# Kernel optimization log

Measured on AMD Instinct MI355X. Metric: run time of the kernel, lower is better.

Reference implementation:

```python
import jax, jax.numpy as jnp
import numpy as np

N_NODES = 50000

def gcn_conv(x, src, dst, W, b, n_nodes):
    # PyG GCNConv: add self-loops, symmetric deg^{-1/2} normalization,
    # linear transform, scatter-add aggregation (source -> target), bias.
    loop = jnp.arange(n_nodes, dtype=src.dtype)
    src2 = jnp.concatenate([src, loop])
    dst2 = jnp.concatenate([dst, loop])
    deg = jax.ops.segment_sum(jnp.ones_like(dst2, dtype=x.dtype), dst2, num_segments=n_nodes)
    dinv = jnp.where(deg > 0, jax.lax.rsqrt(deg), 0.0)
    norm = dinv[src2] * dinv[dst2]  # [E + N]
    h = x @ W                        # [N, out]
    msg = h[src2] * norm[:, None]    # gather + scale
    out = jax.ops.segment_sum(msg, dst2, num_segments=n_nodes)
    return out + b

def setup_inputs() -> dict:
    key = jax.random.key(0)
    k1, k2, k3, k4 = jax.random.split(key, 4)
    x = jax.random.normal(k1, (N_NODES, 64), dtype=jnp.float32)
    edge_index = jax.random.randint(k2, (2, 800000), 0, N_NODES, dtype=jnp.int64)
    # Glorot-ish init for weights
    W1 = jax.random.normal(k3, (64, 128), dtype=jnp.float32) * (1.0 / np.sqrt(64))
    b1 = jnp.zeros((128,), dtype=jnp.float32)
    W2 = jax.random.normal(k4, (128, 8), dtype=jnp.float32) * (1.0 / np.sqrt(128))
    b2 = jnp.zeros((8,), dtype=jnp.float32)
    return {"x": x, "edge_index": edge_index, "W1": W1, "b1": b1, "W2": W2, "b2": b2}

def reference(x, edge_index, W1, b1, W2, b2):
    src, dst = edge_index[0], edge_index[1]
    h = gcn_conv(x, src, dst, W1, b1, N_NODES)
    h = jax.nn.relu(h)
    out = gcn_conv(h, src, dst, W2, b2, N_NODES)
    return out
```

## Files before the change

### kernel.cpp

```cpp
#include <hip/hip_runtime.h>

#define IN1 64
#define MID 128
#define OUT2 8
#define YPAD 136
#define TPAD 68
#define CAP 64

__device__ __forceinline__ unsigned short f2bf(float f) {
    unsigned int u = __float_as_uint(f);
    unsigned int r = (u + 0x7fff + ((u >> 16) & 1)) >> 16;
    return (unsigned short)r;
}
__device__ __forceinline__ float bflo(unsigned int u) { return __uint_as_float(u << 16); }
__device__ __forceinline__ float bfhi(unsigned int u) { return __uint_as_float(u & 0xffff0000u); }

__global__ __launch_bounds__(256) void k_xb(const float4* __restrict__ x4,
                                            ushort4* __restrict__ xb4,
                                            int* __restrict__ cnt, int n16, int N) {
    int gid = blockIdx.x * 256 + (int)threadIdx.x;
    if (gid < N) cnt[gid] = 0;
    if (gid >= n16) return;
    float4 vx = x4[gid];
    ushort4 pv;
    pv.x = f2bf(vx.x); pv.y = f2bf(vx.y);
    pv.z = f2bf(vx.z); pv.w = f2bf(vx.w);
    xb4[gid] = pv;
}

__global__ __launch_bounds__(256) void k_fill(const int* __restrict__ src,
                                              const int* __restrict__ dst,
                                              int* __restrict__ cnt,
                                              unsigned short* __restrict__ col,
                                              int E4, int E, int npx, int slices) {
    int xcd = blockIdx.x & 7;
    int slice = blockIdx.x >> 3;
    int lo = xcd * npx, hi = lo + npx;
    int eps = (E4 + slices - 1) / slices;
    int g0 = slice * eps, g1 = min(E4, g0 + eps);
    int g = g0 + (int)threadIdx.x;
    if (g < g1) {
        int4 dv = ((const int4*)dst)[g];
        int4 sv = ((const int4*)src)[g];
        for (;;) {
            int gn = g + 256;
            bool has = gn < g1;
            int4 dn, sn;
            if (has) { dn = ((const int4*)dst)[gn]; sn = ((const int4*)src)[gn]; }
            if (dv.x >= lo && dv.x < hi) {
                int p = atomicAdd(&cnt[dv.x], 1);
                if (p < CAP) col[dv.x * CAP + p] = (unsigned short)sv.x;
            }
            if (dv.y >= lo && dv.y < hi) {
                int p = atomicAdd(&cnt[dv.y], 1);
                if (p < CAP) col[dv.y * CAP + p] = (unsigned short)sv.y;
            }
            if (dv.z >= lo && dv.z < hi) {
                int p = atomicAdd(&cnt[dv.z], 1);
                if (p < CAP) col[dv.z * CAP + p] = (unsigned short)sv.z;
            }
            if (dv.w >= lo && dv.w < hi) {
                int p = atomicAdd(&cnt[dv.w], 1);
                if (p < CAP) col[dv.w * CAP + p] = (unsigned short)sv.w;
            }
            if (!has) break;
            dv = dn; sv = sn;
            g = gn;
        }
    }
    if (blockIdx.x == 0 && threadIdx.x == 0) {
        for (int e = E4 * 4; e < E; ++e) {
            int d = dst[e];
            int p = atomicAdd(&cnt[d], 1);
            if (p < CAP) col[d * CAP + p] = (unsigned short)src[e];
        }
    }
}

__global__ __launch_bounds__(256) void k_node(const uint4* __restrict__ xb4,
                                              const int* __restrict__ cnt,
                                              const unsigned short* __restrict__ col,
                                              const float* __restrict__ W1,
                                              const float* __restrict__ b1,
                                              const float* __restrict__ W2,
                                              float* __restrict__ z, int n) {
    __shared__ float w2s[MID * OUT2];
    __shared__ float tS[4][8][TPAD];
    __shared__ float yS[4][8][YPAD];

    int t = threadIdx.x;
    ((float4*)w2s)[t] = ((const float4*)W2)[t];

    int lane = t & 63, wave = t >> 6;
    int g = lane >> 3;
    int fl = lane & 7;
    int row0 = blockIdx.x * 32 + wave * 8;
    int row = row0 + g;
    bool valid = row < n;

    float a0=0.f,a1=0.f,a2=0.f,a3=0.f,a4=0.f,a5=0.f,a6=0.f,a7=0.f;
    int deg = 0, base = 0;
    if (valid) {
        int c0 = cnt[row];
        deg = min(c0, CAP);
        base = row * CAP;
        float dself = rsqrtf((float)(c0 + 1));
        uint4 u = xb4[(size_t)row * 8 + fl];
        a0 = dself * bflo(u.x); a1 = dself * bfhi(u.x);
        a2 = dself * bflo(u.y); a3 = dself * bfhi(u.y);
        a4 = dself * bflo(u.z); a5 = dself * bfhi(u.z);
        a6 = dself * bflo(u.w); a7 = dself * bfhi(u.w);
    }
    int cv = (deg >= 8) ? col[base + fl] : 0;
    float dsv = rsqrtf((float)(cnt[cv] + 1));
    int j = 0;
    for (; j + 8 <= deg; j += 8) {
        int cvn = (j + 16 <= deg) ? col[base + j + 8 + fl] : 0;
        float dsn = rsqrtf((float)(cnt[cvn] + 1));
#pragma unroll
        for (int p = 0; p < 8; ++p) {
            int sl = (g << 3) + p;
            int s = __shfl(cv, sl, 64);
            float ds = __shfl(dsv, sl, 64);
            uint4 u = xb4[(size_t)s * 8 + fl];
            a0 = fmaf(ds, bflo(u.x), a0); a1 = fmaf(ds, bfhi(u.x), a1);
            a2 = fmaf(ds, bflo(u.y), a2); a3 = fmaf(ds, bfhi(u.y), a3);
            a4 = fmaf(ds, bflo(u.z), a4); a5 = fmaf(ds, bfhi(u.z), a5);
            a6 = fmaf(ds, bflo(u.w), a6); a7 = fmaf(ds, bfhi(u.w), a7);
        }
        cv = cvn; dsv = dsn;
    }
    int rem = deg - j;
    if (rem > 0) {
        int cvr = col[base + min(j + fl, CAP - 1)];
        float dsr = rsqrtf((float)(cnt[cvr] + 1));
#pragma unroll
        for (int p = 0; p < 8; ++p) {
            if (p < rem) {
                int sl = (g << 3) + p;
                int s = __shfl(cvr, sl, 64);
                float ds = __shfl(dsr, sl, 64);
                uint4 u = xb4[(size_t)s * 8 + fl];
                a0 = fmaf(ds, bflo(u.x), a0); a1 = fmaf(ds, bfhi(u.x), a1);
                a2 = fmaf(ds, bflo(u.y), a2); a3 = fmaf(ds, bfhi(u.y), a3);
                a4 = fmaf(ds, bflo(u.z), a4); a5 = fmaf(ds, bfhi(u.z), a5);
                a6 = fmaf(ds, bflo(u.w), a6); a7 = fmaf(ds, bfhi(u.w), a7);
            }
        }
    }
    {
        float4 w0 = {a0, a1, a2, a3};
        float4 w1v = {a4, a5, a6, a7};
        *(float4*)&tS[wave][g][8 * fl] = w0;
        *(float4*)&tS[wave][g][8 * fl + 4] = w1v;
    }

    float dnd[8];
#pragma unroll
    for (int k = 0; k < 8; ++k) {
        int ck = cnt[min(row0 + k, n - 1)];
        dnd[k] = rsqrtf((float)(ck + 1));
    }

    float ya[8], yb[8];
#pragma unroll
    for (int i = 0; i < 8; ++i) { ya[i] = 0.f; yb[i] = 0.f; }
#pragma unroll 2
    for (int k4 = 0; k4 < IN1; k4 += 4) {
        float4 tv[8];
#pragma unroll
        for (int nd = 0; nd < 8; ++nd) tv[nd] = *(const float4*)&tS[wave][nd][k4];
#pragma unroll
        for (int kk = 0; kk < 4; ++kk) {
            int k = k4 + kk;
            float wa = W1[k * MID + lane];
            float wb = W1[k * MID + lane + 64];
#pragma unroll
            for (int nd = 0; nd < 8; ++nd) {
                float e = (&tv[nd].x)[kk];
                ya[nd] = fmaf(e, wa, ya[nd]);
                yb[nd] = fmaf(e, wb, yb[nd]);
            }
        }
    }
    float bl = b1[lane], bh = b1[lane + 64];
#pragma unroll
    for (int nd = 0; nd < 8; ++nd) {
        yS[wave][nd][lane] = fmaxf(fmaf(ya[nd], dnd[nd], bl), 0.f);
        yS[wave][nd][lane + 64] = fmaxf(fmaf(yb[nd], dnd[nd], bh), 0.f);
    }

    __syncthreads();

    int nd2 = lane >> 3, ch = lane & 7;
    float p[OUT2];
#pragma unroll
    for (int c = 0; c < OUT2; ++c) p[c] = 0.0f;
#pragma unroll
    for (int kk = 0; kk < 16; ++kk) {
        int k = kk * 8 + ch;
        float yk = yS[wave][nd2][k];
        float4 wlo = *(const float4*)&w2s[k * OUT2];
        float4 whi = *(const float4*)&w2s[k * OUT2 + 4];
        p[0] = fmaf(yk, wlo.x, p[0]); p[1] = fmaf(yk, wlo.y, p[1]);
        p[2] = fmaf(yk, wlo.z, p[2]); p[3] = fmaf(yk, wlo.w, p[3]);
        p[4] = fmaf(yk, whi.x, p[4]); p[5] = fmaf(yk, whi.y, p[5]);
        p[6] = fmaf(yk, whi.z, p[6]); p[7] = fmaf(yk, whi.w, p[7]);
    }
#pragma unroll
    for (int off = 1; off < 8; off <<= 1) {
#pragma unroll
        for (int c = 0; c < OUT2; ++c) p[c] += __shfl_xor(p[c], off, 64);
    }
    int rw = row0 + nd2;
    if (rw < n) {
        z[(size_t)rw * OUT2 + ch] = p[ch] * dnd[nd2];
    }
}

__global__ __launch_bounds__(256) void k_gather2(const int* __restrict__ cnt,
                                                 const unsigned short* __restrict__ col,
                                                 const float* __restrict__ z,
                                                 const float* __restrict__ b2,
                                                 float* __restrict__ out, int n) {
    int t = threadIdx.x, lane = t & 63, wave = t >> 6;
    int node = blockIdx.x * 4 + wave;
    if (node >= n) return;
    int nb = lane >> 3, c = lane & 7;
    float acc = (nb == 0) ? z[(size_t)node * OUT2 + c] : 0.0f;
    int c0 = cnt[node];
    int deg = min(c0, CAP);
    int base = node * CAP;
    int j = nb;
    if (j + 8 < deg) {
        int s0 = col[base + j], s1 = col[base + j + 8];
        for (; j + 8 < deg;) {
            int jn = j + 16;
            int t0 = 0, t1 = 0;
            bool has = jn + 8 < deg;
            if (has) { t0 = col[base + jn]; t1 = col[base + jn + 8]; }
            acc += z[(size_t)s0 * OUT2 + c] + z[(size_t)s1 * OUT2 + c];
            j = jn;
            if (!has) break;
            s0 = t0; s1 = t1;
        }
    }
    if (j < deg) acc += z[(size_t)col[base + j] * OUT2 + c];
#pragma unroll
    for (int off = 8; off < 64; off <<= 1) acc += __shfl_xor(acc, off, 64);
    if (lane < OUT2) out[(size_t)node * OUT2 + lane] = fmaf(acc, rsqrtf((float)(c0 + 1)), b2[lane]);
}

extern "C" void kernel_launch(void* const* d_in, const int* in_sizes, int n_in,
                              void* d_out, int out_size, void* d_ws, size_t ws_size,
                              hipStream_t stream) {
    const float* x  = (const float*)d_in[0];
    const int*   ei = (const int*)d_in[1];
    const float* W1 = (const float*)d_in[2];
    const float* b1 = (const float*)d_in[3];
    const float* W2 = (const float*)d_in[4];
    const float* b2 = (const float*)d_in[5];
    float* out = (float*)d_out;

    int N = in_sizes[0] / IN1;
    int E = in_sizes[1] / 2;
    const int* src = ei;
    const int* dst = ei + E;

    int* cnt = (int*)d_ws;
    unsigned short* col = (unsigned short*)(cnt + N);
    float* z = (float*)(col + (size_t)N * CAP);
    unsigned short* xb = (unsigned short*)(z + (size_t)N * OUT2);

    const int B = 256;
    int E4 = E / 4;
    int npx = (N + 7) / 8;
    int slices = 256;
    int n16 = N * 16;

    k_xb<<<(n16 + B - 1) / B, B, 0, stream>>>((const float4*)x, (ushort4*)xb, cnt, n16, N);
    k_fill<<<slices * 8, B, 0, stream>>>(src, dst, cnt, col, E4, E, npx, slices);
    k_node<<<(N + 31) / 32, 256, 0, stream>>>((const uint4*)xb, cnt, col, W1, b1, W2, z, N);
    k_gather2<<<(N + 3) / 4, 256, 0, stream>>>(cnt, col, z, b2, out, N);
}
```

Measured before the change: 170.9 us.

## Precompute degree normalization in fill kernel and simplify gather loop

The last block per XCD slice of the fill kernel, found with an atomic done counter, computes dinv = rsqrt(cnt+1) for its node range. The node and gather kernels then read dinv directly instead of recomputing rsqrt from cnt for every neighbor. The shuffle-based software prefetch of neighbor indices in the aggregation loop is replaced by direct per-neighbor col and dinv loads. W2 is now read from global memory instead of shared memory, which lets the block-wide barrier go, and YPAD shrinks. In exchange it adds an atomic and threadfence at the end of the fill kernel, and it may lose the latency hiding the old prefetch provided.

```diff
diff --git a/kernel.cpp b/kernel.cpp
--- a/kernel.cpp
+++ b/kernel.cpp
@@ -3,7 +3,7 @@
 #define IN1 64
 #define MID 128
 #define OUT2 8
-#define YPAD 136
+#define YPAD 132
 #define TPAD 68
 #define CAP 64
 
@@ -17,9 +17,11 @@
 
 __global__ __launch_bounds__(256) void k_xb(const float4* __restrict__ x4,
                                             ushort4* __restrict__ xb4,
-                                            int* __restrict__ cnt, int n16, int N) {
+                                            int* __restrict__ cnt,
+                                            int* __restrict__ done, int n16, int N) {
     int gid = blockIdx.x * 256 + (int)threadIdx.x;
     if (gid < N) cnt[gid] = 0;
+    if (gid < 8) done[gid] = 0;
     if (gid >= n16) return;
     float4 vx = x4[gid];
     ushort4 pv;
@@ -32,10 +34,12 @@
                                               const int* __restrict__ dst,
                                               int* __restrict__ cnt,
                                               unsigned short* __restrict__ col,
-                                              int E4, int E, int npx, int slices) {
+                                              int* __restrict__ done,
+                                              float* __restrict__ dinv,
+                                              int E4, int E, int npx, int slices, int N) {
     int xcd = blockIdx.x & 7;
     int slice = blockIdx.x >> 3;
-    int lo = xcd * npx, hi = lo + npx;
+    int lo = xcd * npx, hi = min(lo + npx, N);
     int eps = (E4 + slices - 1) / slices;
     int g0 = slice * eps, g1 = min(E4, g0 + eps);
     int g = g0 + (int)threadIdx.x;
@@ -75,22 +79,28 @@
             if (p < CAP) col[d * CAP + p] = (unsigned short)src[e];
         }
     }
+    __threadfence();
+    __shared__ int sT;
+    if (threadIdx.x == 0) sT = atomicAdd(&done[xcd], 1);
+    __syncthreads();
+    if (sT == slices - 1) {
+        for (int i = lo + (int)threadIdx.x; i < hi; i += 256)
+            dinv[i] = rsqrtf((float)(cnt[i] + 1));
+    }
 }
 
 __global__ __launch_bounds__(256) void k_node(const uint4* __restrict__ xb4,
                                               const int* __restrict__ cnt,
                                               const unsigned short* __restrict__ col,
+                                              const float* __restrict__ dinv,
                                               const float* __restrict__ W1,
                                               const float* __restrict__ b1,
                                               const float* __restrict__ W2,
                                               float* __restrict__ z, int n) {
-    __shared__ float w2s[MID * OUT2];
     __shared__ float tS[4][8][TPAD];
     __shared__ float yS[4][8][YPAD];
 
     int t = threadIdx.x;
-    ((float4*)w2s)[t] = ((const float4*)W2)[t];
-
     int lane = t & 63, wave = t >> 6;
     int g = lane >> 3;
     int fl = lane & 7;
@@ -101,45 +111,35 @@
     float a0=0.f,a1=0.f,a2=0.f,a3=0.f,a4=0.f,a5=0.f,a6=0.f,a7=0.f;
     int deg = 0, base = 0;
     if (valid) {
-        int c0 = cnt[row];
-        deg = min(c0, CAP);
+        deg = min(cnt[row], CAP);
         base = row * CAP;
-        float dself = rsqrtf((float)(c0 + 1));
+        float dself = dinv[row];
         uint4 u = xb4[(size_t)row * 8 + fl];
         a0 = dself * bflo(u.x); a1 = dself * bfhi(u.x);
         a2 = dself * bflo(u.y); a3 = dself * bfhi(u.y);
         a4 = dself * bflo(u.z); a5 = dself * bfhi(u.z);
         a6 = dself * bflo(u.w); a7 = dself * bfhi(u.w);
     }
-    int cv = (deg >= 8) ? col[base + fl] : 0;
-    float dsv = rsqrtf((float)(cnt[cv] + 1));
     int j = 0;
     for (; j + 8 <= deg; j += 8) {
-        int cvn = (j + 16 <= deg) ? col[base + j + 8 + fl] : 0;
-        float dsn = rsqrtf((float)(cnt[cvn] + 1));
 #pragma unroll
         for (int p = 0; p < 8; ++p) {
-            int sl = (g << 3) + p;
-            int s = __shfl(cv, sl, 64);
-            float ds = __shfl(dsv, sl, 64);
+            int s = (int)col[base + j + p];
+            float ds = dinv[s];
             uint4 u = xb4[(size_t)s * 8 + fl];
             a0 = fmaf(ds, bflo(u.x), a0); a1 = fmaf(ds, bfhi(u.x), a1);
             a2 = fmaf(ds, bflo(u.y), a2); a3 = fmaf(ds, bfhi(u.y), a3);
             a4 = fmaf(ds, bflo(u.z), a4); a5 = fmaf(ds, bfhi(u.z), a5);
             a6 = fmaf(ds, bflo(u.w), a6); a7 = fmaf(ds, bfhi(u.w), a7);
         }
-        cv = cvn; dsv = dsn;
     }
     int rem = deg - j;
     if (rem > 0) {
-        int cvr = col[base + min(j + fl, CAP - 1)];
-        float dsr = rsqrtf((float)(cnt[cvr] + 1));
 #pragma unroll
         for (int p = 0; p < 8; ++p) {
             if (p < rem) {
-                int sl = (g << 3) + p;
-                int s = __shfl(cvr, sl, 64);
-                float ds = __shfl(dsr, sl, 64);
+                int s = (int)col[base + j + p];
+                float ds = dinv[s];
                 uint4 u = xb4[(size_t)s * 8 + fl];
                 a0 = fmaf(ds, bflo(u.x), a0); a1 = fmaf(ds, bfhi(u.x), a1);
                 a2 = fmaf(ds, bflo(u.y), a2); a3 = fmaf(ds, bfhi(u.y), a3);
@@ -157,10 +157,7 @@
 
     float dnd[8];
 #pragma unroll
-    for (int k = 0; k < 8; ++k) {
-        int ck = cnt[min(row0 + k, n - 1)];
-        dnd[k] = rsqrtf((float)(ck + 1));
-    }
+    for (int k = 0; k < 8; ++k) dnd[k] = dinv[min(row0 + k, n - 1)];
 
     float ya[8], yb[8];
 #pragma unroll
@@ -190,9 +187,8 @@
         yS[wave][nd][lane + 64] = fmaxf(fmaf(yb[nd], dnd[nd], bh), 0.f);
     }
 
-    __syncthreads();
-
     int nd2 = lane >> 3, ch = lane & 7;
+    const float4* W24 = (const float4*)W2;
     float p[OUT2];
 #pragma unroll
     for (int c = 0; c < OUT2; ++c) p[c] = 0.0f;
@@ -200,8 +196,8 @@
     for (int kk = 0; kk < 16; ++kk) {
         int k = kk * 8 + ch;
         float yk = yS[wave][nd2][k];
-        float4 wlo = *(const float4*)&w2s[k * OUT2];
-        float4 whi = *(const float4*)&w2s[k * OUT2 + 4];
+        float4 wlo = W24[k * 2];
+        float4 whi = W24[k * 2 + 1];
         p[0] = fmaf(yk, wlo.x, p[0]); p[1] = fmaf(yk, wlo.y, p[1]);
         p[2] = fmaf(yk, wlo.z, p[2]); p[3] = fmaf(yk, wlo.w, p[3]);
         p[4] = fmaf(yk, whi.x, p[4]); p[5] = fmaf(yk, whi.y, p[5]);
@@ -221,6 +217,7 @@
 __global__ __launch_bounds__(256) void k_gather2(const int* __restrict__ cnt,
                                                  const unsigned short* __restrict__ col,
                                                  const float* __restrict__ z,
+                                                 const float* __restrict__ dinv,
                                                  const float* __restrict__ b2,
                                                  float* __restrict__ out, int n) {
     int t = threadIdx.x, lane = t & 63, wave = t >> 6;
@@ -228,8 +225,7 @@
     if (node >= n) return;
     int nb = lane >> 3, c = lane & 7;
     float acc = (nb == 0) ? z[(size_t)node * OUT2 + c] : 0.0f;
-    int c0 = cnt[node];
-    int deg = min(c0, CAP);
+    int deg = min(cnt[node], CAP);
     int base = node * CAP;
     int j = nb;
     if (j + 8 < deg) {
@@ -248,7 +244,7 @@
     if (j < deg) acc += z[(size_t)col[base + j] * OUT2 + c];
 #pragma unroll
     for (int off = 8; off < 64; off <<= 1) acc += __shfl_xor(acc, off, 64);
-    if (lane < OUT2) out[(size_t)node * OUT2 + lane] = fmaf(acc, rsqrtf((float)(c0 + 1)), b2[lane]);
+    if (lane < OUT2) out[(size_t)node * OUT2 + lane] = fmaf(acc, dinv[node], b2[lane]);
 }
 
 extern "C" void kernel_launch(void* const* d_in, const int* in_sizes, int n_in,
@@ -268,7 +264,9 @@
     const int* dst = ei + E;
 
     int* cnt = (int*)d_ws;
-    unsigned short* col = (unsigned short*)(cnt + N);
+    int* done = cnt + N;
+    float* dinv = (float*)(done + 8);
+    unsigned short* col = (unsigned short*)(dinv + N);
     float* z = (float*)(col + (size_t)N * CAP);
     unsigned short* xb = (unsigned short*)(z + (size_t)N * OUT2);
 
@@ -278,8 +276,8 @@
     int slices = 256;
     int n16 = N * 16;
 
-    k_xb<<<(n16 + B - 1) / B, B, 0, stream>>>((const float4*)x, (ushort4*)xb, cnt, n16, N);
-    k_fill<<<slices * 8, B, 0, stream>>>(src, dst, cnt, col, E4, E, npx, slices);
-    k_node<<<(N + 31) / 32, 256, 0, stream>>>((const uint4*)xb, cnt, col, W1, b1, W2, z, N);
-    k_gather2<<<(N + 3) / 4, 256, 0, stream>>>(cnt, col, z, b2, out, N);
-}
+    k_xb<<<(n16 + B - 1) / B, B, 0, stream>>>((const float4*)x, (ushort4*)xb, cnt, done, n16, N);
+    k_fill<<<slices * 8, B, 0, stream>>>(src, dst, cnt, col, done, dinv, E4, E, npx, slices, N);
+    k_node<<<(N + 31) / 32, 256, 0, stream>>>((const uint4*)xb, cnt, col, dinv, W1, b1, W2, z, N);
+    k_gather2<<<(N + 3) / 4, 256, 0, stream>>>(cnt, col, z, dinv, b2, out, N);
+}
```

Measured after the change: 407.6 us. 2.39x slower.
